# Performance work log

Hardware: AMD Instinct MI355X
Metric: run time of the kernel (lower is better)

## Reference

```python
import jax, jax.numpy as jnp
import numpy as np

N_NODES = 50000
HEADS = 4
NEG_SLOPE = 0.2


def _gat_conv(x, src, dst, W, a_src, a_dst, b):
    """PyG GATConv (concat=True, add_self_loops already applied to src/dst).
    x: [N, F_in], W: [F_in, H*C], a_src/a_dst: [H, C], b: [H*C]."""
    N = x.shape[0]
    HC = W.shape[1]
    C = HC // HEADS
    h = (x @ W).reshape(N, HEADS, C)                       # [N, H, C]
    alpha_s = (h * a_src[None]).sum(-1)                    # [N, H]
    alpha_d = (h * a_dst[None]).sum(-1)                    # [N, H]
    e = jax.nn.leaky_relu(alpha_s[src] + alpha_d[dst], NEG_SLOPE)  # [E, H]
    # segment softmax over incoming edges of each destination node
    m = jax.ops.segment_max(e, dst, num_segments=N)        # [N, H]
    ex = jnp.exp(e - m[dst])
    denom = jax.ops.segment_sum(ex, dst, num_segments=N)   # [N, H]
    alpha = ex / (denom[dst] + 1e-16)                      # [E, H]
    msg = h[src] * alpha[:, :, None]                       # [E, H, C]
    out = jax.ops.segment_sum(msg, dst, num_segments=N)    # [N, H, C]
    return out.reshape(N, HC) + b


def _glorot(key, shape, fan):
    lim = float(np.sqrt(6.0 / fan))
    return jax.random.uniform(key, shape, jnp.float32, -lim, lim)


def setup_inputs() -> dict:
    key = jax.random.key(0)
    ks = jax.random.split(key, 16)
    N, E, F_in, Hid, Out = N_NODES, 800000, 128, 256, 256
    x = jax.random.normal(ks[0], (N, F_in), jnp.float32)
    edge_index = jax.random.randint(ks[1], (2, E), 0, N, jnp.int64)
    C1, C2, C3 = Hid // HEADS, Hid // HEADS, Out // HEADS
    d = {"x": x, "edge_index": edge_index}
    dims = [(F_in, HEADS * C1, C1), (Hid, HEADS * C2, C2), (Hid, HEADS * C3, C3)]
    for i, (fi, fo, c) in enumerate(dims, 1):
        d[f"W{i}"] = _glorot(ks[3 * i], (fi, fo), fi + fo)
        d[f"a_src{i}"] = _glorot(ks[3 * i + 1], (HEADS, c), HEADS * c)
        d[f"a_dst{i}"] = _glorot(ks[3 * i + 2], (HEADS, c), HEADS * c)
        d[f"b{i}"] = jnp.zeros((fo,), jnp.float32)
    return d


def reference(x, edge_index, W1, a_src1, a_dst1, b1, W2, a_src2, a_dst2, b2, W3, a_src3, a_dst3, b3):
    N = x.shape[0]
    loops = jnp.arange(N, dtype=edge_index.dtype)
    src = jnp.concatenate([edge_index[0], loops])  # PyG add_self_loops=True
    dst = jnp.concatenate([edge_index[1], loops])
    h = _gat_conv(x, src, dst, W1, a_src1, a_dst1, b1)
    h = jax.nn.relu(h)  # dropout inert in eval mode
    h = _gat_conv(h, src, dst, W2, a_src2, a_dst2, b2)
    h = jax.nn.relu(h)
    return _gat_conv(h, src, dst, W3, a_src3, a_dst3, b3)
```

## Files before the change

kernel.cpp:

```cpp
#include <hip/hip_runtime.h>
#include <hip/hip_bf16.h>

typedef unsigned short u16;
typedef __attribute__((ext_vector_type(8))) short short8;
typedef __attribute__((ext_vector_type(4))) float f32x4;

#define HC 256
#define NHEAD 4

__device__ __forceinline__ u16 f2b_rne(float v) {
  __hip_bfloat16 b = __float2bfloat16(v);
  union { __hip_bfloat16 b; u16 u; } cv; cv.b = b; return cv.u;
}

__device__ __forceinline__ void w_split_store(const float* W, u16* Th, u16* Tl,
                                              int K, int off) {
  int k = off >> 8, n = off & 255;
  float v = W[off];
  unsigned bits = __float_as_uint(v);
  u16 hi = (u16)(bits >> 16);
  float hf = __uint_as_float((unsigned)hi << 16);
  u16 lo = f2b_rne(v - hf);
  Th[n * K + k] = hi;
  Tl[n * K + k] = lo;
}

__global__ void convert_w3(const float* __restrict__ W1, const float* __restrict__ W2,
                           const float* __restrict__ W3,
                           u16* __restrict__ Th1, u16* __restrict__ Tl1,
                           u16* __restrict__ Th2, u16* __restrict__ Tl2,
                           u16* __restrict__ Th3, u16* __restrict__ Tl3) {
  int id = blockIdx.x * 256 + threadIdx.x;
  const int S1 = 128 * 256, S2 = 256 * 256;
  if (id < S1) w_split_store(W1, Th1, Tl1, 128, id);
  else if (id < S1 + S2) w_split_store(W2, Th2, Tl2, 256, id - S1);
  else if (id < S1 + 2 * S2) w_split_store(W3, Th3, Tl3, 256, id - S1 - S2);
}

#define GBM 128
#define GBN 128
#define GBK 64

__global__ __launch_bounds__(256, 2) void gemm_mfma(
    const float* __restrict__ A, const u16* __restrict__ Bth,
    const u16* __restrict__ Btl, float* __restrict__ C,
    const float* __restrict__ a_src, const float* __restrict__ a_dst,
    float* __restrict__ AS, float* __restrict__ AD, int M, int K, int nMb) {
  __shared__ u16 AH[128 * 64], AL[128 * 64], BH[128 * 64], BL[128 * 64];
  const int tid = threadIdx.x;
  const int lane = tid & 63;
  const int wave = tid >> 6;
  const int wm = (wave & 1) * 64;
  const int wn = (wave >> 1) * 64;

  const int bid = blockIdx.x;
  const int g = bid >> 4;
  const int r = bid & 15;
  const int base = g * 8;
  const int rem = nMb - base;
  int bmi, bni;
  if (rem >= 8) { bmi = base + (r & 7); bni = r >> 3; }
  else          { bmi = base + (r % rem); bni = r / rem; }
  const int bm = bmi * GBM;
  const int bn = bni * GBN;

  const int srow = tid >> 1;
  const int skh  = (tid & 1) * 32;

  f32x4 acc[4][4] = {};

  const int agm = (bm + srow < M) ? (bm + srow) : (M - 1);

  for (int bk = 0; bk < K; bk += GBK) {
    float4 a0[4], a1[4];
    const float* arow = A + (size_t)agm * K + bk + skh;
#pragma unroll
    for (int u = 0; u < 4; ++u) {
      a0[u] = ((const float4*)arow)[2 * u];
      a1[u] = ((const float4*)arow)[2 * u + 1];
    }
    short8 sbh[4], sbl[4];
    const u16* bhrow = Bth + (size_t)(bn + srow) * K + bk + skh;
    const u16* blrow = Btl + (size_t)(bn + srow) * K + bk + skh;
#pragma unroll
    for (int u = 0; u < 4; ++u) {
      sbh[u] = *(const short8*)(bhrow + 8 * u);
      sbl[u] = *(const short8*)(blrow + 8 * u);
    }
    __syncthreads();
#pragma unroll
    for (int u = 0; u < 4; ++u) {
      int idx = (srow * 64 + skh + u * 8) ^ ((srow & 7) << 3);
      float va[8] = {a0[u].x, a0[u].y, a0[u].z, a0[u].w,
                     a1[u].x, a1[u].y, a1[u].z, a1[u].w};
      short8 hi, lo;
#pragma unroll
      for (int j = 0; j < 8; ++j) {
        unsigned bits = __float_as_uint(va[j]);
        u16 h = (u16)(bits >> 16);
        float hf = __uint_as_float((unsigned)h << 16);
        u16 l = f2b_rne(va[j] - hf);
        ((short*)&hi)[j] = (short)h;
        ((short*)&lo)[j] = (short)l;
      }
      *(short8*)&AH[idx] = hi;
      *(short8*)&AL[idx] = lo;
      *(short8*)&BH[idx] = sbh[u];
      *(short8*)&BL[idx] = sbl[u];
    }
    __syncthreads();
#pragma unroll
    for (int ks = 0; ks < 2; ++ks) {
      const int k0 = ks * 32 + (lane >> 4) * 8;
      short8 fah[4], fal[4], fbh[4], fbl[4];
#pragma unroll
      for (int mt = 0; mt < 4; ++mt) {
        int rr = wm + mt * 16 + (lane & 15);
        int idx = (rr * 64 + k0) ^ ((rr & 7) << 3);
        fah[mt] = *(const short8*)&AH[idx];
        fal[mt] = *(const short8*)&AL[idx];
      }
#pragma unroll
      for (int nt = 0; nt < 4; ++nt) {
        int rr = wn + nt * 16 + (lane & 15);
        int idx = (rr * 64 + k0) ^ ((rr & 7) << 3);
        fbh[nt] = *(const short8*)&BH[idx];
        fbl[nt] = *(const short8*)&BL[idx];
      }
#pragma unroll
      for (int mt = 0; mt < 4; ++mt)
#pragma unroll
        for (int nt = 0; nt < 4; ++nt) {
          acc[mt][nt] = __builtin_amdgcn_mfma_f32_16x16x32_bf16(
              fbh[nt], fah[mt], acc[mt][nt], 0, 0, 0);
          acc[mt][nt] = __builtin_amdgcn_mfma_f32_16x16x32_bf16(
              fbh[nt], fal[mt], acc[mt][nt], 0, 0, 0);
          acc[mt][nt] = __builtin_amdgcn_mfma_f32_16x16x32_bf16(
              fbl[nt], fah[mt], acc[mt][nt], 0, 0, 0);
        }
    }
  }
  const int headq = (bn + wn) >> 6;
  float4 sa[4], da[4];
#pragma unroll
  for (int nt = 0; nt < 4; ++nt) {
    sa[nt] = ((const float4*)a_src)[headq * 16 + nt * 4 + (lane >> 4)];
    da[nt] = ((const float4*)a_dst)[headq * 16 + nt * 4 + (lane >> 4)];
  }
#pragma unroll
  for (int mt = 0; mt < 4; ++mt) {
    const int row = bm + wm + mt * 16 + (lane & 15);
    float ps = 0.f, pd = 0.f;
#pragma unroll
    for (int nt = 0; nt < 4; ++nt) {
      ps += acc[mt][nt][0] * sa[nt].x + acc[mt][nt][1] * sa[nt].y +
            acc[mt][nt][2] * sa[nt].z + acc[mt][nt][3] * sa[nt].w;
      pd += acc[mt][nt][0] * da[nt].x + acc[mt][nt][1] * da[nt].y +
            acc[mt][nt][2] * da[nt].z + acc[mt][nt][3] * da[nt].w;
    }
    ps += __shfl_xor(ps, 16); ps += __shfl_xor(ps, 32);
    pd += __shfl_xor(pd, 16); pd += __shfl_xor(pd, 32);
    if (row < M) {
      float* cp = C + (size_t)row * HC + bn + wn + (lane >> 4) * 4;
#pragma unroll
      for (int nt = 0; nt < 4; ++nt)
        *(f32x4*)(cp + nt * 16) = acc[mt][nt];
      if ((lane >> 4) == 0) {
        AS[row * NHEAD + headq] = ps;
        AD[row * NHEAD + headq] = pd;
      }
    }
  }
}

__device__ __forceinline__ float comp4(float4 v, int i) {
  return (i == 0) ? v.x : (i == 1) ? v.y : (i == 2) ? v.z : v.w;
}

__global__ __launch_bounds__(512) void aggregate_kernel(
    const float* __restrict__ h, const float* __restrict__ as_g,
    const float* __restrict__ ad_g, const int* __restrict__ row_ptr,
    const int* __restrict__ csr_src, const float* __restrict__ bias,
    float* __restrict__ out, int relu_flag, int N) {
  __shared__ float4 lacc[4][64];
  __shared__ float lsum[4][64];
  const int wid = threadIdx.x >> 6;
  const int lane = threadIdx.x & 63;
  const int p = wid >> 1;
  const int q = wid & 1;
  const int n = blockIdx.x * 4 + p;
  const int nc = (n < N) ? n : (N - 1);
  const int head = lane >> 4;
  const float4* __restrict__ h4 = (const float4*)h;
  const float4* __restrict__ as4 = (const float4*)as_g;

  const int beg = row_ptr[nc];
  const int end = row_ptr[nc + 1];

  float4 m4 = make_float4(-1e30f, -1e30f, -1e30f, -1e30f);
  for (int j = beg + lane; j < end; j += 64) {
    float4 a = as4[csr_src[j]];
    m4.x = fmaxf(m4.x, a.x); m4.y = fmaxf(m4.y, a.y);
    m4.z = fmaxf(m4.z, a.z); m4.w = fmaxf(m4.w, a.w);
  }
#pragma unroll
  for (int off = 32; off > 0; off >>= 1) {
    m4.x = fmaxf(m4.x, __shfl_xor(m4.x, off));
    m4.y = fmaxf(m4.y, __shfl_xor(m4.y, off));
    m4.z = fmaxf(m4.z, __shfl_xor(m4.z, off));
    m4.w = fmaxf(m4.w, __shfl_xor(m4.w, off));
  }
  const float ad = comp4(((const float4*)ad_g)[nc], head);
  float mm = ad + comp4(m4, head);
  mm = (mm >= 0.f) ? mm : 0.2f * mm;

  float l = 0.f;
  float4 acc = make_float4(0.f, 0.f, 0.f, 0.f);
  for (int j0 = beg + q * 8; j0 < end; j0 += 16) {
    int s[8];
    float ae[8];
    float4 hv[8];
#pragma unroll
    for (int u = 0; u < 8; ++u) {
      int j = j0 + u;
      s[u] = csr_src[(j < end) ? j : (end - 1)];
    }
#pragma unroll
    for (int u = 0; u < 8; ++u) ae[u] = as_g[s[u] * NHEAD + head];
#pragma unroll
    for (int u = 0; u < 8; ++u) hv[u] = h4[(size_t)s[u] * 64 + lane];
#pragma unroll
    for (int u = 0; u < 8; ++u) {
      float e = ae[u] + ad;
      e = (e >= 0.f) ? e : 0.2f * e;
      float pw = __expf(e - mm);
      pw = (j0 + u < end) ? pw : 0.f;
      l += pw;
      acc.x = fmaf(pw, hv[u].x, acc.x);
      acc.y = fmaf(pw, hv[u].y, acc.y);
      acc.z = fmaf(pw, hv[u].z, acc.z);
      acc.w = fmaf(pw, hv[u].w, acc.w);
    }
  }
  if (q == 1) { lacc[p][lane] = acc; lsum[p][lane] = l; }
  __syncthreads();
  if (q == 0 && n < N) {
    float4 a2 = lacc[p][lane];
    acc.x += a2.x; acc.y += a2.y; acc.z += a2.z; acc.w += a2.w;
    l += lsum[p][lane];
    const float inv = 1.f / (l + 1e-16f);
    float4 b4 = ((const float4*)bias)[lane];
    float4 o;
    o.x = acc.x * inv + b4.x; o.y = acc.y * inv + b4.y;
    o.z = acc.z * inv + b4.z; o.w = acc.w * inv + b4.w;
    if (relu_flag) {
      o.x = fmaxf(o.x, 0.f); o.y = fmaxf(o.y, 0.f);
      o.z = fmaxf(o.z, 0.f); o.w = fmaxf(o.w, 0.f);
    }
    ((float4*)out)[(size_t)n * 64 + lane] = o;
  }
}

__global__ void detect_kernel(const int* __restrict__ ei32, int* flag) {
  const int t = threadIdx.x;
  int bad = 0;
#pragma unroll
  for (int r = 0; r < 4; ++r) {
    int i = r * 64 + t;
    if (ei32[2 * i + 1] != 0) bad = 1;
  }
#pragma unroll
  for (int off = 32; off > 0; off >>= 1) bad |= __shfl_down(bad, off);
  if (t == 0) *flag = bad ? 0 : 1;
}

__device__ inline void edge_pair(const int* __restrict__ ei32,
                                 const long long* __restrict__ ei64, int is64,
                                 int e, int E, int& src, int& dst) {
  if (e < E) {
    if (is64) { src = (int)ei64[e]; dst = (int)ei64[(size_t)E + e]; }
    else      { src = ei32[e];      dst = ei32[(size_t)E + e]; }
  } else {
    src = dst = e - E;
  }
}

__global__ void count_kernel(const int* __restrict__ ei32, const int* __restrict__ flag,
                             int* __restrict__ cnt, int E, int Nn) {
  int e = blockIdx.x * blockDim.x + threadIdx.x;
  if (e >= E + Nn) return;
  int is64 = *flag;
  int src, dst;
  edge_pair(ei32, (const long long*)ei32, is64, e, E, src, dst);
  atomicAdd(&cnt[dst], 1);
}

__global__ void scatter_kernel(const int* __restrict__ ei32, const int* __restrict__ flag,
                               int* __restrict__ cursor, int* __restrict__ csr_src,
                               int E, int Nn) {
  int e = blockIdx.x * blockDim.x + threadIdx.x;
  if (e >= E + Nn) return;
  int is64 = *flag;
  int src, dst;
  edge_pair(ei32, (const long long*)ei32, is64, e, E, src, dst);
  int pos = atomicAdd(&cursor[dst], 1);
  csr_src[pos] = src;
}

__global__ __launch_bounds__(256) void scan_blocks(
    const int* __restrict__ cnt, int* __restrict__ local,
    int* __restrict__ partials, int Nn) {
  __shared__ int swave[4];
  const int t = threadIdx.x, lane = t & 63, w = t >> 6;
  const int idx = blockIdx.x * 256 + t;
  int v = (idx < Nn) ? cnt[idx] : 0;
  int x = v;
#pragma unroll
  for (int off = 1; off < 64; off <<= 1) {
    int y = __shfl_up(x, off);
    if (lane >= off) x += y;
  }
  if (lane == 63) swave[w] = x;
  __syncthreads();
  int wofs = 0;
#pragma unroll
  for (int i = 0; i < 3; ++i) wofs += (i < w) ? swave[i] : 0;
  if (idx < Nn) local[idx] = wofs + x - v;
  if (t == 255) partials[blockIdx.x] = wofs + x;
}

__global__ __launch_bounds__(256) void scan_partials(
    int* __restrict__ partials, int nb, int* __restrict__ total_out) {
  __shared__ int swave[4];
  const int t = threadIdx.x, lane = t & 63, w = t >> 6;
  int v = (t < nb) ? partials[t] : 0;
  int x = v;
#pragma unroll
  for (int off = 1; off < 64; off <<= 1) {
    int y = __shfl_up(x, off);
    if (lane >= off) x += y;
  }
  if (lane == 63) swave[w] = x;
  __syncthreads();
  int wofs = 0;
#pragma unroll
  for (int i = 0; i < 3; ++i) wofs += (i < w) ? swave[i] : 0;
  int excl = wofs + x - v;
  if (t < nb) partials[t] = excl;
  if (t == nb - 1) *total_out = excl + v;
}

__global__ void add_offsets(const int* __restrict__ local,
                            const int* __restrict__ partials,
                            int* __restrict__ row_ptr, int* __restrict__ cursor,
                            int Nn) {
  const int idx = blockIdx.x * 256 + threadIdx.x;
  if (idx < Nn) {
    int v = local[idx] + partials[blockIdx.x];
    row_ptr[idx] = v;
    cursor[idx] = v;
  }
}

static inline size_t align_up(size_t v) { return (v + 255) & ~(size_t)255; }

extern "C" void kernel_launch(void* const* d_in, const int* in_sizes, int n_in,
                              void* d_out, int out_size, void* d_ws, size_t ws_size,
                              hipStream_t stream) {
  const float* x      = (const float*)d_in[0];
  const int*   ei32   = (const int*)d_in[1];
  const float* W1     = (const float*)d_in[2];
  const float* asrc1  = (const float*)d_in[3];
  const float* adst1  = (const float*)d_in[4];
  const float* b1     = (const float*)d_in[5];
  const float* W2     = (const float*)d_in[6];
  const float* asrc2  = (const float*)d_in[7];
  const float* adst2  = (const float*)d_in[8];
  const float* b2     = (const float*)d_in[9];
  const float* W3     = (const float*)d_in[10];
  const float* asrc3  = (const float*)d_in[11];
  const float* adst3  = (const float*)d_in[12];
  const float* b3     = (const float*)d_in[13];

  const int N = in_sizes[0] / 128;
  const int E = in_sizes[1] / 2;
  const int ET = E + N;
  float* out = (float*)d_out;
  const int nb = (N + 255) / 256;

  char* w = (char*)d_ws;
  float* H       = (float*)w; w += align_up((size_t)N * HC * sizeof(float));
  float* AS      = (float*)w; w += align_up((size_t)N * NHEAD * sizeof(float));
  float* AD      = (float*)w; w += align_up((size_t)N * NHEAD * sizeof(float));
  int*   cnt     = (int*)w;   w += align_up((size_t)N * sizeof(int));
  int*   local   = (int*)w;   w += align_up((size_t)N * sizeof(int));
  int*   row_ptr = (int*)w;   w += align_up((size_t)(N + 1) * sizeof(int));
  int*   cursor  = (int*)w;   w += align_up((size_t)(N + 1) * sizeof(int));
  int*   parts   = (int*)w;   w += align_up(256 * sizeof(int));
  int*   csr_src = (int*)w;   w += align_up((size_t)ET * sizeof(int));
  u16*   Wth1    = (u16*)w;   w += align_up((size_t)128 * 256 * sizeof(u16));
  u16*   Wtl1    = (u16*)w;   w += align_up((size_t)128 * 256 * sizeof(u16));
  u16*   Wth2    = (u16*)w;   w += align_up((size_t)256 * 256 * sizeof(u16));
  u16*   Wtl2    = (u16*)w;   w += align_up((size_t)256 * 256 * sizeof(u16));
  u16*   Wth3    = (u16*)w;   w += align_up((size_t)256 * 256 * sizeof(u16));
  u16*   Wtl3    = (u16*)w;   w += align_up((size_t)256 * 256 * sizeof(u16));
  int*   flag    = (int*)w;   w += align_up(sizeof(int));

  convert_w3<<<(128 * 256 + 2 * 256 * 256 + 255) / 256, 256, 0, stream>>>(
      W1, W2, W3, Wth1, Wtl1, Wth2, Wtl2, Wth3, Wtl3);
  hipMemsetAsync(cnt, 0, (size_t)N * sizeof(int), stream);
  detect_kernel<<<1, 64, 0, stream>>>(ei32, flag);
  count_kernel<<<(ET + 255) / 256, 256, 0, stream>>>(ei32, flag, cnt, E, N);
  scan_blocks<<<nb, 256, 0, stream>>>(cnt, local, parts, N);
  scan_partials<<<1, 256, 0, stream>>>(parts, nb, row_ptr + N);
  add_offsets<<<nb, 256, 0, stream>>>(local, parts, row_ptr, cursor, N);
  scatter_kernel<<<(ET + 255) / 256, 256, 0, stream>>>(ei32, flag, cursor, csr_src, E, N);

  const int nMb = (N + GBM - 1) / GBM;
  const int gemm_blocks = nMb * 2;
  const int ablk = (N + 3) / 4;

  gemm_mfma<<<gemm_blocks, 256, 0, stream>>>(x, Wth1, Wtl1, H, asrc1, adst1, AS, AD, N, 128, nMb);
  aggregate_kernel<<<ablk, 512, 0, stream>>>(H, AS, AD, row_ptr, csr_src, b1, out, 1, N);

  gemm_mfma<<<gemm_blocks, 256, 0, stream>>>(out, Wth2, Wtl2, H, asrc2, adst2, AS, AD, N, 256, nMb);
  aggregate_kernel<<<ablk, 512, 0, stream>>>(H, AS, AD, row_ptr, csr_src, b2, out, 1, N);

  gemm_mfma<<<gemm_blocks, 256, 0, stream>>>(out, Wth3, Wtl3, H, asrc3, adst3, AS, AD, N, 256, nMb);
  aggregate_kernel<<<ablk, 512, 0, stream>>>(H, AS, AD, row_ptr, csr_src, b3, out, 0, N);
}
```

Before: 598.4 us.

## Aggregate raw features before projection in layer one, fold attention vectors into W1

For the first GAT layer, the attention logits are computed straight from x by folding W1 into a_src/a_dst, giving a 128x4 vector per head. The softmax-weighted neighbour sum then runs on the 128-wide input features, producing one aggregate per head, and a per-head GEMM projects that aggregate and applies bias and ReLU. Gathers drop from 256 to 128 floats per edge, but the GEMM input grows to four times N x 128, which costs extra memory traffic and workspace. The aggregate kernel is also changed from two waves per node with an LDS reduction to one wave per node.

```diff
diff --git a/kernel.cpp b/kernel.cpp
--- a/kernel.cpp
+++ b/kernel.cpp
@@ -35,6 +35,268 @@
   if (id < S1) w_split_store(W1, Th1, Tl1, 128, id);
   else if (id < S1 + S2) w_split_store(W2, Th2, Tl2, 256, id - S1);
   else if (id < S1 + 2 * S2) w_split_store(W3, Th3, Tl3, 256, id - S1 - S2);
+}
+
+__global__ __launch_bounds__(256) void fold_wa(
+    const float* __restrict__ W1, const float* __restrict__ a_src,
+    const float* __restrict__ a_dst, float* __restrict__ wa_s,
+    float* __restrict__ wa_d) {
+  int id = blockIdx.x * 256 + threadIdx.x;
+  if (id >= 512) return;
+  int c = id >> 2, h = id & 3;
+  const float* wrow = W1 + c * 256 + h * 64;
+  const float* as = a_src + h * 64;
+  const float* ad = a_dst + h * 64;
+  float ss = 0.f, sd = 0.f;
+#pragma unroll 8
+  for (int cc = 0; cc < 64; ++cc) {
+    float w = wrow[cc];
+    ss += w * as[cc];
+    sd += w * ad[cc];
+  }
+  wa_s[c * 4 + h] = ss;
+  wa_d[c * 4 + h] = sd;
+}
+
+__global__ __launch_bounds__(256) void alpha_x(
+    const float* __restrict__ x, const float* __restrict__ wa_s,
+    const float* __restrict__ wa_d, float* __restrict__ AS,
+    float* __restrict__ AD, int N) {
+  const int wave = threadIdx.x >> 6;
+  const int lane = threadIdx.x & 63;
+  const int n = blockIdx.x * 4 + wave;
+  if (n >= N) return;
+  float2 xv = ((const float2*)x)[(size_t)n * 64 + lane];
+  float4 sA = ((const float4*)wa_s)[2 * lane];
+  float4 sB = ((const float4*)wa_s)[2 * lane + 1];
+  float4 dA = ((const float4*)wa_d)[2 * lane];
+  float4 dB = ((const float4*)wa_d)[2 * lane + 1];
+  float ps[4], pd[4];
+  ps[0] = xv.x * sA.x + xv.y * sB.x;  pd[0] = xv.x * dA.x + xv.y * dB.x;
+  ps[1] = xv.x * sA.y + xv.y * sB.y;  pd[1] = xv.x * dA.y + xv.y * dB.y;
+  ps[2] = xv.x * sA.z + xv.y * sB.z;  pd[2] = xv.x * dA.z + xv.y * dB.z;
+  ps[3] = xv.x * sA.w + xv.y * sB.w;  pd[3] = xv.x * dA.w + xv.y * dB.w;
+#pragma unroll
+  for (int off = 1; off < 64; off <<= 1) {
+#pragma unroll
+    for (int h = 0; h < 4; ++h) {
+      ps[h] += __shfl_xor(ps[h], off);
+      pd[h] += __shfl_xor(pd[h], off);
+    }
+  }
+  if (lane == 0) {
+#pragma unroll
+    for (int h = 0; h < 4; ++h) {
+      AS[n * NHEAD + h] = ps[h];
+      AD[n * NHEAD + h] = pd[h];
+    }
+  }
+}
+
+__device__ __forceinline__ float lky(float e) {
+  return (e >= 0.f) ? e : 0.2f * e;
+}
+
+__global__ __launch_bounds__(256) void aggregate_x4(
+    const float* __restrict__ x, const float* __restrict__ as_g,
+    const float* __restrict__ ad_g, const int* __restrict__ row_ptr,
+    const int* __restrict__ csr_src, float* __restrict__ xagg, int N) {
+  const int wave = threadIdx.x >> 6;
+  const int lane = threadIdx.x & 63;
+  const int n = blockIdx.x * 4 + wave;
+  if (n >= N) return;
+  const float2* __restrict__ x2 = (const float2*)x;
+  const float4* __restrict__ as4 = (const float4*)as_g;
+
+  const int beg = row_ptr[n];
+  const int end = row_ptr[n + 1];
+
+  float4 m4 = make_float4(-1e30f, -1e30f, -1e30f, -1e30f);
+  for (int j = beg + lane; j < end; j += 64) {
+    float4 a = as4[csr_src[j]];
+    m4.x = fmaxf(m4.x, a.x); m4.y = fmaxf(m4.y, a.y);
+    m4.z = fmaxf(m4.z, a.z); m4.w = fmaxf(m4.w, a.w);
+  }
+#pragma unroll
+  for (int off = 32; off > 0; off >>= 1) {
+    m4.x = fmaxf(m4.x, __shfl_xor(m4.x, off));
+    m4.y = fmaxf(m4.y, __shfl_xor(m4.y, off));
+    m4.z = fmaxf(m4.z, __shfl_xor(m4.z, off));
+    m4.w = fmaxf(m4.w, __shfl_xor(m4.w, off));
+  }
+  const float4 ad4 = ((const float4*)ad_g)[n];
+  float4 mm4;
+  mm4.x = lky(ad4.x + m4.x);
+  mm4.y = lky(ad4.y + m4.y);
+  mm4.z = lky(ad4.z + m4.z);
+  mm4.w = lky(ad4.w + m4.w);
+
+  float4 l4 = make_float4(0.f, 0.f, 0.f, 0.f);
+  float2 ac0 = make_float2(0.f, 0.f), ac1 = ac0, ac2 = ac0, ac3 = ac0;
+  for (int j0 = beg; j0 < end; j0 += 8) {
+    int s[8];
+    float4 av[8];
+    float2 xv[8];
+#pragma unroll
+    for (int u = 0; u < 8; ++u) {
+      int j = j0 + u;
+      s[u] = csr_src[(j < end) ? j : (end - 1)];
+    }
+#pragma unroll
+    for (int u = 0; u < 8; ++u) av[u] = as4[s[u]];
+#pragma unroll
+    for (int u = 0; u < 8; ++u) xv[u] = x2[(size_t)s[u] * 64 + lane];
+#pragma unroll
+    for (int u = 0; u < 8; ++u) {
+      const bool live = (j0 + u < end);
+      float4 p;
+      p.x = __expf(lky(av[u].x + ad4.x) - mm4.x);
+      p.y = __expf(lky(av[u].y + ad4.y) - mm4.y);
+      p.z = __expf(lky(av[u].z + ad4.z) - mm4.z);
+      p.w = __expf(lky(av[u].w + ad4.w) - mm4.w);
+      p.x = live ? p.x : 0.f; p.y = live ? p.y : 0.f;
+      p.z = live ? p.z : 0.f; p.w = live ? p.w : 0.f;
+      l4.x += p.x; l4.y += p.y; l4.z += p.z; l4.w += p.w;
+      ac0.x = fmaf(p.x, xv[u].x, ac0.x); ac0.y = fmaf(p.x, xv[u].y, ac0.y);
+      ac1.x = fmaf(p.y, xv[u].x, ac1.x); ac1.y = fmaf(p.y, xv[u].y, ac1.y);
+      ac2.x = fmaf(p.z, xv[u].x, ac2.x); ac2.y = fmaf(p.z, xv[u].y, ac2.y);
+      ac3.x = fmaf(p.w, xv[u].x, ac3.x); ac3.y = fmaf(p.w, xv[u].y, ac3.y);
+    }
+  }
+  const float i0 = 1.f / (l4.x + 1e-16f);
+  const float i1 = 1.f / (l4.y + 1e-16f);
+  const float i2 = 1.f / (l4.z + 1e-16f);
+  const float i3 = 1.f / (l4.w + 1e-16f);
+  float2* __restrict__ o2 = (float2*)xagg;
+  const size_t plane = (size_t)N * 64;
+  const size_t base = (size_t)n * 64 + lane;
+  o2[0 * plane + base] = make_float2(ac0.x * i0, ac0.y * i0);
+  o2[1 * plane + base] = make_float2(ac1.x * i1, ac1.y * i1);
+  o2[2 * plane + base] = make_float2(ac2.x * i2, ac2.y * i2);
+  o2[3 * plane + base] = make_float2(ac3.x * i3, ac3.y * i3);
+}
+
+__global__ __launch_bounds__(256, 2) void gemm_mfma_h(
+    const float* __restrict__ Aall, const u16* __restrict__ Bth,
+    const u16* __restrict__ Btl, float* __restrict__ C,
+    const float* __restrict__ bias, int M) {
+  __shared__ u16 AH[128 * 64], AL[128 * 64], BH[64 * 64], BL[64 * 64];
+  const int tid = threadIdx.x;
+  const int lane = tid & 63;
+  const int wave = tid >> 6;
+  const int wm = (wave & 1) * 64;
+  const int wn = (wave >> 1) * 32;
+  const int head = blockIdx.y;
+  const int bm = blockIdx.x * 128;
+
+  const float* A = Aall + (size_t)head * M * 128;
+  const u16* bth = Bth + head * 64 * 128;
+  const u16* btl = Btl + head * 64 * 128;
+
+  const int srow = tid >> 1;
+  const int skh  = (tid & 1) * 32;
+  const int bcol = tid >> 2;
+  const int bkq  = (tid & 3) * 16;
+
+  f32x4 acc[4][2] = {};
+  const int agm = (bm + srow < M) ? (bm + srow) : (M - 1);
+
+  for (int bk = 0; bk < 128; bk += 64) {
+    float4 a0[4], a1[4];
+    const float* arow = A + (size_t)agm * 128 + bk + skh;
+#pragma unroll
+    for (int u = 0; u < 4; ++u) {
+      a0[u] = ((const float4*)arow)[2 * u];
+      a1[u] = ((const float4*)arow)[2 * u + 1];
+    }
+    short8 sbh[2], sbl[2];
+    {
+      const u16* p = bth + bcol * 128 + bk + bkq;
+      sbh[0] = *(const short8*)p;
+      sbh[1] = *(const short8*)(p + 8);
+      const u16* q = btl + bcol * 128 + bk + bkq;
+      sbl[0] = *(const short8*)q;
+      sbl[1] = *(const short8*)(q + 8);
+    }
+    __syncthreads();
+#pragma unroll
+    for (int u = 0; u < 4; ++u) {
+      int idx = (srow * 64 + skh + u * 8) ^ ((srow & 7) << 3);
+      float va[8] = {a0[u].x, a0[u].y, a0[u].z, a0[u].w,
+                     a1[u].x, a1[u].y, a1[u].z, a1[u].w};
+      short8 hi, lo;
+#pragma unroll
+      for (int j = 0; j < 8; ++j) {
+        unsigned bits = __float_as_uint(va[j]);
+        u16 h = (u16)(bits >> 16);
+        float hf = __uint_as_float((unsigned)h << 16);
+        u16 l = f2b_rne(va[j] - hf);
+        ((short*)&hi)[j] = (short)h;
+        ((short*)&lo)[j] = (short)l;
+      }
+      *(short8*)&AH[idx] = hi;
+      *(short8*)&AL[idx] = lo;
+    }
+    {
+      int i0 = (bcol * 64 + bkq) ^ ((bcol & 7) << 3);
+      int i1 = (bcol * 64 + bkq + 8) ^ ((bcol & 7) << 3);
+      *(short8*)&BH[i0] = sbh[0];
+      *(short8*)&BH[i1] = sbh[1];
+      *(short8*)&BL[i0] = sbl[0];
+      *(short8*)&BL[i1] = sbl[1];
+    }
+    __syncthreads();
+#pragma unroll
+    for (int ks = 0; ks < 2; ++ks) {
+      const int k0 = ks * 32 + (lane >> 4) * 8;
+      short8 fah[4], fal[4], fbh[2], fbl[2];
+#pragma unroll
+      for (int mt = 0; mt < 4; ++mt) {
+        int rr = wm + mt * 16 + (lane & 15);
+        int idx = (rr * 64 + k0) ^ ((rr & 7) << 3);
+        fah[mt] = *(const short8*)&AH[idx];
+        fal[mt] = *(const short8*)&AL[idx];
+      }
+#pragma unroll
+      for (int nt = 0; nt < 2; ++nt) {
+        int rr = wn + nt * 16 + (lane & 15);
+        int idx = (rr * 64 + k0) ^ ((rr & 7) << 3);
+        fbh[nt] = *(const short8*)&BH[idx];
+        fbl[nt] = *(const short8*)&BL[idx];
+      }
+#pragma unroll
+      for (int mt = 0; mt < 4; ++mt)
+#pragma unroll
+        for (int nt = 0; nt < 2; ++nt) {
+          acc[mt][nt] = __builtin_amdgcn_mfma_f32_16x16x32_bf16(
+              fbh[nt], fah[mt], acc[mt][nt], 0, 0, 0);
+          acc[mt][nt] = __builtin_amdgcn_mfma_f32_16x16x32_bf16(
+              fbh[nt], fal[mt], acc[mt][nt], 0, 0, 0);
+          acc[mt][nt] = __builtin_amdgcn_mfma_f32_16x16x32_bf16(
+              fbl[nt], fah[mt], acc[mt][nt], 0, 0, 0);
+        }
+    }
+  }
+  float4 b4[2];
+#pragma unroll
+  for (int nt = 0; nt < 2; ++nt)
+    b4[nt] = ((const float4*)bias)[head * 16 + (wn >> 2) + nt * 4 + (lane >> 4)];
+#pragma unroll
+  for (int mt = 0; mt < 4; ++mt) {
+    const int row = bm + wm + mt * 16 + (lane & 15);
+    if (row < M) {
+      float* cp = C + (size_t)row * HC + head * 64 + wn + (lane >> 4) * 4;
+#pragma unroll
+      for (int nt = 0; nt < 2; ++nt) {
+        f32x4 v = acc[mt][nt];
+        v[0] = fmaxf(v[0] + b4[nt].x, 0.f);
+        v[1] = fmaxf(v[1] + b4[nt].y, 0.f);
+        v[2] = fmaxf(v[2] + b4[nt].z, 0.f);
+        v[3] = fmaxf(v[3] + b4[nt].w, 0.f);
+        *(f32x4*)(cp + nt * 16) = v;
+      }
+    }
+  }
 }
 
 #define GBM 128
@@ -68,7 +330,6 @@
   const int skh  = (tid & 1) * 32;
 
   f32x4 acc[4][4] = {};
-
   const int agm = (bm + srow < M) ? (bm + srow) : (M - 1);
 
   for (int bk = 0; bk < K; bk += GBK) {
@@ -177,25 +438,21 @@
   return (i == 0) ? v.x : (i == 1) ? v.y : (i == 2) ? v.z : v.w;
 }
 
-__global__ __launch_bounds__(512) void aggregate_kernel(
+__global__ __launch_bounds__(256) void aggregate_kernel(
     const float* __restrict__ h, const float* __restrict__ as_g,
     const float* __restrict__ ad_g, const int* __restrict__ row_ptr,
     const int* __restrict__ csr_src, const float* __restrict__ bias,
     float* __restrict__ out, int relu_flag, int N) {
-  __shared__ float4 lacc[4][64];
-  __shared__ float lsum[4][64];
-  const int wid = threadIdx.x >> 6;
+  const int wave = threadIdx.x >> 6;
   const int lane = threadIdx.x & 63;
-  const int p = wid >> 1;
-  const int q = wid & 1;
-  const int n = blockIdx.x * 4 + p;
-  const int nc = (n < N) ? n : (N - 1);
+  const int n = blockIdx.x * 4 + wave;
+  if (n >= N) return;
   const int head = lane >> 4;
   const float4* __restrict__ h4 = (const float4*)h;
   const float4* __restrict__ as4 = (const float4*)as_g;
 
-  const int beg = row_ptr[nc];
-  const int end = row_ptr[nc + 1];
+  const int beg = row_ptr[n];
+  const int end = row_ptr[n + 1];
 
   float4 m4 = make_float4(-1e30f, -1e30f, -1e30f, -1e30f);
   for (int j = beg + lane; j < end; j += 64) {
@@ -210,13 +467,12 @@
     m4.z = fmaxf(m4.z, __shfl_xor(m4.z, off));
     m4.w = fmaxf(m4.w, __shfl_xor(m4.w, off));
   }
-  const float ad = comp4(((const float4*)ad_g)[nc], head);
-  float mm = ad + comp4(m4, head);
-  mm = (mm >= 0.f) ? mm : 0.2f * mm;
+  const float ad = comp4(((const float4*)ad_g)[n], head);
+  float mm = lky(ad + comp4(m4, head));
 
   float l = 0.f;
   float4 acc = make_float4(0.f, 0.f, 0.f, 0.f);
-  for (int j0 = beg + q * 8; j0 < end; j0 += 16) {
+  for (int j0 = beg; j0 < end; j0 += 8) {
     int s[8];
     float ae[8];
     float4 hv[8];
@@ -231,34 +487,25 @@
     for (int u = 0; u < 8; ++u) hv[u] = h4[(size_t)s[u] * 64 + lane];
 #pragma unroll
     for (int u = 0; u < 8; ++u) {
-      float e = ae[u] + ad;
-      e = (e >= 0.f) ? e : 0.2f * e;
-      float pw = __expf(e - mm);
-      pw = (j0 + u < end) ? pw : 0.f;
-      l += pw;
-      acc.x = fmaf(pw, hv[u].x, acc.x);
-      acc.y = fmaf(pw, hv[u].y, acc.y);
-      acc.z = fmaf(pw, hv[u].z, acc.z);
-      acc.w = fmaf(pw, hv[u].w, acc.w);
-    }
-  }
-  if (q == 1) { lacc[p][lane] = acc; lsum[p][lane] = l; }
-  __syncthreads();
-  if (q == 0 && n < N) {
-    float4 a2 = lacc[p][lane];
-    acc.x += a2.x; acc.y += a2.y; acc.z += a2.z; acc.w += a2.w;
-    l += lsum[p][lane];
-    const float inv = 1.f / (l + 1e-16f);
-    float4 b4 = ((const float4*)bias)[lane];
-    float4 o;
-    o.x = acc.x * inv + b4.x; o.y = acc.y * inv + b4.y;
-    o.z = acc.z * inv + b4.z; o.w = acc.w * inv + b4.w;
-    if (relu_flag) {
-      o.x = fmaxf(o.x, 0.f); o.y = fmaxf(o.y, 0.f);
-      o.z = fmaxf(o.z, 0.f); o.w = fmaxf(o.w, 0.f);
-    }
-    ((float4*)out)[(size_t)n * 64 + lane] = o;
-  }
+      float p = __expf(lky(ae[u] + ad) - mm);
+      p = (j0 + u < end) ? p : 0.f;
+      l += p;
+      acc.x = fmaf(p, hv[u].x, acc.x);
+      acc.y = fmaf(p, hv[u].y, acc.y);
+      acc.z = fmaf(p, hv[u].z, acc.z);
+      acc.w = fmaf(p, hv[u].w, acc.w);
+    }
+  }
+  const float inv = 1.f / (l + 1e-16f);
+  float4 b4 = ((const float4*)bias)[lane];
+  float4 o;
+  o.x = acc.x * inv + b4.x; o.y = acc.y * inv + b4.y;
+  o.z = acc.z * inv + b4.z; o.w = acc.w * inv + b4.w;
+  if (relu_flag) {
+    o.x = fmaxf(o.x, 0.f); o.y = fmaxf(o.y, 0.f);
+    o.z = fmaxf(o.z, 0.f); o.w = fmaxf(o.w, 0.f);
+  }
+  ((float4*)out)[(size_t)n * 64 + lane] = o;
 }
 
 __global__ void detect_kernel(const int* __restrict__ ei32, int* flag) {
@@ -389,9 +636,12 @@
   const int nb = (N + 255) / 256;
 
   char* w = (char*)d_ws;
-  float* H       = (float*)w; w += align_up((size_t)N * HC * sizeof(float));
+  float* XAGG    = (float*)w;
+  float* H       = (float*)w; w += align_up((size_t)N * 512 * sizeof(float));
   float* AS      = (float*)w; w += align_up((size_t)N * NHEAD * sizeof(float));
   float* AD      = (float*)w; w += align_up((size_t)N * NHEAD * sizeof(float));
+  float* WA1S    = (float*)w; w += align_up((size_t)128 * 4 * sizeof(float));
+  float* WA1D    = (float*)w; w += align_up((size_t)128 * 4 * sizeof(float));
   int*   cnt     = (int*)w;   w += align_up((size_t)N * sizeof(int));
   int*   local   = (int*)w;   w += align_up((size_t)N * sizeof(int));
   int*   row_ptr = (int*)w;   w += align_up((size_t)(N + 1) * sizeof(int));
@@ -408,6 +658,7 @@
 
   convert_w3<<<(128 * 256 + 2 * 256 * 256 + 255) / 256, 256, 0, stream>>>(
       W1, W2, W3, Wth1, Wtl1, Wth2, Wtl2, Wth3, Wtl3);
+  fold_wa<<<2, 256, 0, stream>>>(W1, asrc1, adst1, WA1S, WA1D);
   hipMemsetAsync(cnt, 0, (size_t)N * sizeof(int), stream);
   detect_kernel<<<1, 64, 0, stream>>>(ei32, flag);
   count_kernel<<<(ET + 255) / 256, 256, 0, stream>>>(ei32, flag, cnt, E, N);
@@ -420,12 +671,15 @@
   const int gemm_blocks = nMb * 2;
   const int ablk = (N + 3) / 4;
 
-  gemm_mfma<<<gemm_blocks, 256, 0, stream>>>(x, Wth1, Wtl1, H, asrc1, adst1, AS, AD, N, 128, nMb);
-  aggregate_kernel<<<ablk, 512, 0, stream>>>(H, AS, AD, row_ptr, csr_src, b1, out, 1, N);
-
-  gemm_mfma<<<gemm_blocks, 256, 0, stream>>>(out, Wth2, Wtl2, H, asrc2, adst2, AS, AD, N, 256, nMb);
-  aggregate_kernel<<<ablk, 512, 0, stream>>>(H, AS, AD, row_ptr, csr_src, b2, out, 1, N);
-
-  gemm_mfma<<<gemm_blocks, 256, 0, stream>>>(out, Wth3, Wtl3, H, asrc3, adst3, AS, AD, N, 256, nMb);
-  aggregate_kernel<<<ablk, 512, 0, stream>>>(H, AS, AD, row_ptr, csr_src, b3, out, 0, N);
-}
+  alpha_x<<<ablk, 256, 0, stream>>>(x, WA1S, WA1D, AS, AD, N);
+  aggregate_x4<<<ablk, 256, 0, stream>>>(x, AS, AD, row_ptr, csr_src, XAGG, N);
+  gemm_mfma_h<<<dim3(nMb, 4), 256, 0, stream>>>(XAGG, Wth1, Wtl1, out, b1, N);
+
+  gemm_mfma<<<gemm_blocks, 256, 0, stream>>>(out, Wth2, Wtl2, H,
+      asrc2, adst2, AS, AD, N, 256, nMb);
+  aggregate_kernel<<<ablk, 256, 0, stream>>>(H, AS, AD, row_ptr, csr_src, b2, out, 1, N);
+
+  gemm_mfma<<<gemm_blocks, 256, 0, stream>>>(out, Wth3, Wtl3, H,
+      asrc3, adst3, AS, AD, N, 256, nMb);
+  aggregate_kernel<<<ablk, 256, 0, stream>>>(H, AS, AD, row_ptr, csr_src, b3, out, 0, N);
+}
```

Result: no change. 608.7 us (+1.7%).

## Split GAT aggregation into softmax stats pass and column-sliced aggregate

Applied to the files above, without the earlier changes.

Moves the per-node softmax max and denominator into a separate softmax_stats kernel, so the aggregation no longer needs a running sum or a cross-wave LDS reduction. The aggregation now runs 8 blocks per group of 4 nodes, each handling a 32-column slice (one head half). Within a wave, the two lane halves take alternating edges and are combined with a shuffle. This makes the feature gathers narrower and likely more L2-friendly, and raises parallelism. The cost is an extra kernel launch per layer and the edge index and attention scores being re-read once per slice.

```diff
diff --git a/kernel.cpp b/kernel.cpp
--- a/kernel.cpp
+++ b/kernel.cpp
@@ -35,6 +35,14 @@
   if (id < S1) w_split_store(W1, Th1, Tl1, 128, id);
   else if (id < S1 + S2) w_split_store(W2, Th2, Tl2, 256, id - S1);
   else if (id < S1 + 2 * S2) w_split_store(W3, Th3, Tl3, 256, id - S1 - S2);
+}
+
+__device__ __forceinline__ float lky(float e) {
+  return (e >= 0.f) ? e : 0.2f * e;
+}
+
+__device__ __forceinline__ float comp4(float4 v, int i) {
+  return (i == 0) ? v.x : (i == 1) ? v.y : (i == 2) ? v.z : v.w;
 }
 
 #define GBM 128
@@ -68,7 +76,6 @@
   const int skh  = (tid & 1) * 32;
 
   f32x4 acc[4][4] = {};
-
   const int agm = (bm + srow < M) ? (bm + srow) : (M - 1);
 
   for (int bk = 0; bk < K; bk += GBK) {
@@ -173,29 +180,17 @@
   }
 }
 
-__device__ __forceinline__ float comp4(float4 v, int i) {
-  return (i == 0) ? v.x : (i == 1) ? v.y : (i == 2) ? v.z : v.w;
-}
-
-__global__ __launch_bounds__(512) void aggregate_kernel(
-    const float* __restrict__ h, const float* __restrict__ as_g,
-    const float* __restrict__ ad_g, const int* __restrict__ row_ptr,
-    const int* __restrict__ csr_src, const float* __restrict__ bias,
-    float* __restrict__ out, int relu_flag, int N) {
-  __shared__ float4 lacc[4][64];
-  __shared__ float lsum[4][64];
-  const int wid = threadIdx.x >> 6;
+__global__ __launch_bounds__(256) void softmax_stats(
+    const float* __restrict__ as_g, const float* __restrict__ ad_g,
+    const int* __restrict__ row_ptr, const int* __restrict__ csr_src,
+    float* __restrict__ MM, float* __restrict__ INVL, int N) {
+  const int wave = threadIdx.x >> 6;
   const int lane = threadIdx.x & 63;
-  const int p = wid >> 1;
-  const int q = wid & 1;
-  const int n = blockIdx.x * 4 + p;
-  const int nc = (n < N) ? n : (N - 1);
-  const int head = lane >> 4;
-  const float4* __restrict__ h4 = (const float4*)h;
+  const int n = blockIdx.x * 4 + wave;
+  if (n >= N) return;
   const float4* __restrict__ as4 = (const float4*)as_g;
-
-  const int beg = row_ptr[nc];
-  const int end = row_ptr[nc + 1];
+  const int beg = row_ptr[n];
+  const int end = row_ptr[n + 1];
 
   float4 m4 = make_float4(-1e30f, -1e30f, -1e30f, -1e30f);
   for (int j = beg + lane; j < end; j += 64) {
@@ -210,54 +205,88 @@
     m4.z = fmaxf(m4.z, __shfl_xor(m4.z, off));
     m4.w = fmaxf(m4.w, __shfl_xor(m4.w, off));
   }
-  const float ad = comp4(((const float4*)ad_g)[nc], head);
-  float mm = ad + comp4(m4, head);
-  mm = (mm >= 0.f) ? mm : 0.2f * mm;
-
-  float l = 0.f;
-  float4 acc = make_float4(0.f, 0.f, 0.f, 0.f);
-  for (int j0 = beg + q * 8; j0 < end; j0 += 16) {
+  const float4 ad4 = ((const float4*)ad_g)[n];
+  float4 mm4;
+  mm4.x = lky(ad4.x + m4.x);
+  mm4.y = lky(ad4.y + m4.y);
+  mm4.z = lky(ad4.z + m4.z);
+  mm4.w = lky(ad4.w + m4.w);
+
+  float4 l4 = make_float4(0.f, 0.f, 0.f, 0.f);
+  for (int j = beg + lane; j < end; j += 64) {
+    float4 a = as4[csr_src[j]];
+    l4.x += __expf(lky(a.x + ad4.x) - mm4.x);
+    l4.y += __expf(lky(a.y + ad4.y) - mm4.y);
+    l4.z += __expf(lky(a.z + ad4.z) - mm4.z);
+    l4.w += __expf(lky(a.w + ad4.w) - mm4.w);
+  }
+#pragma unroll
+  for (int off = 32; off > 0; off >>= 1) {
+    l4.x += __shfl_xor(l4.x, off);
+    l4.y += __shfl_xor(l4.y, off);
+    l4.z += __shfl_xor(l4.z, off);
+    l4.w += __shfl_xor(l4.w, off);
+  }
+  if (lane == 0) {
+    ((float4*)MM)[n] = mm4;
+    float4 inv;
+    inv.x = 1.f / (l4.x + 1e-16f);
+    inv.y = 1.f / (l4.y + 1e-16f);
+    inv.z = 1.f / (l4.z + 1e-16f);
+    inv.w = 1.f / (l4.w + 1e-16f);
+    ((float4*)INVL)[n] = inv;
+  }
+}
+
+__global__ __launch_bounds__(256) void aggregate_sliced(
+    const float* __restrict__ h, const float* __restrict__ as_g,
+    const float* __restrict__ ad_g, const float* __restrict__ MM,
+    const float* __restrict__ INVL, const int* __restrict__ row_ptr,
+    const int* __restrict__ csr_src, const float* __restrict__ bias,
+    float* __restrict__ out, int relu_flag, int N) {
+  const int q = blockIdx.x & 7;
+  const int ng = blockIdx.x >> 3;
+  const int wave = threadIdx.x >> 6;
+  const int lane = threadIdx.x & 63;
+  const int n = ng * 4 + wave;
+  if (n >= N) return;
+  const int head = q >> 1;
+  const int epar = lane >> 5;
+  const int c = lane & 31;
+
+  const int beg = row_ptr[n];
+  const int end = row_ptr[n + 1];
+  const float ad = ad_g[n * NHEAD + head];
+  const float mm = MM[n * NHEAD + head];
+  const float il = INVL[n * NHEAD + head];
+  const float* __restrict__ hsl = h + q * 32 + c;
+
+  float acc = 0.f;
+  for (int j0 = beg; j0 < end; j0 += 16) {
     int s[8];
     float ae[8];
-    float4 hv[8];
+    float hv[8];
 #pragma unroll
     for (int u = 0; u < 8; ++u) {
-      int j = j0 + u;
+      int j = j0 + 2 * u + epar;
       s[u] = csr_src[(j < end) ? j : (end - 1)];
     }
 #pragma unroll
     for (int u = 0; u < 8; ++u) ae[u] = as_g[s[u] * NHEAD + head];
 #pragma unroll
-    for (int u = 0; u < 8; ++u) hv[u] = h4[(size_t)s[u] * 64 + lane];
+    for (int u = 0; u < 8; ++u) hv[u] = hsl[(size_t)s[u] * HC];
 #pragma unroll
     for (int u = 0; u < 8; ++u) {
-      float e = ae[u] + ad;
-      e = (e >= 0.f) ? e : 0.2f * e;
-      float pw = __expf(e - mm);
-      pw = (j0 + u < end) ? pw : 0.f;
-      l += pw;
-      acc.x = fmaf(pw, hv[u].x, acc.x);
-      acc.y = fmaf(pw, hv[u].y, acc.y);
-      acc.z = fmaf(pw, hv[u].z, acc.z);
-      acc.w = fmaf(pw, hv[u].w, acc.w);
-    }
-  }
-  if (q == 1) { lacc[p][lane] = acc; lsum[p][lane] = l; }
-  __syncthreads();
-  if (q == 0 && n < N) {
-    float4 a2 = lacc[p][lane];
-    acc.x += a2.x; acc.y += a2.y; acc.z += a2.z; acc.w += a2.w;
-    l += lsum[p][lane];
-    const float inv = 1.f / (l + 1e-16f);
-    float4 b4 = ((const float4*)bias)[lane];
-    float4 o;
-    o.x = acc.x * inv + b4.x; o.y = acc.y * inv + b4.y;
-    o.z = acc.z * inv + b4.z; o.w = acc.w * inv + b4.w;
-    if (relu_flag) {
-      o.x = fmaxf(o.x, 0.f); o.y = fmaxf(o.y, 0.f);
-      o.z = fmaxf(o.z, 0.f); o.w = fmaxf(o.w, 0.f);
-    }
-    ((float4*)out)[(size_t)n * 64 + lane] = o;
+      float p = __expf(lky(ae[u] + ad) - mm);
+      p = (j0 + 2 * u + epar < end) ? p : 0.f;
+      acc = fmaf(p, hv[u], acc);
+    }
+  }
+  acc += __shfl_xor(acc, 32);
+  if (epar == 0) {
+    float o = acc * il + bias[q * 32 + c];
+    if (relu_flag) o = fmaxf(o, 0.f);
+    out[(size_t)n * HC + q * 32 + c] = o;
   }
 }
 
@@ -392,6 +421,8 @@
   float* H       = (float*)w; w += align_up((size_t)N * HC * sizeof(float));
   float* AS      = (float*)w; w += align_up((size_t)N * NHEAD * sizeof(float));
   float* AD      = (float*)w; w += align_up((size_t)N * NHEAD * sizeof(float));
+  float* MM      = (float*)w; w += align_up((size_t)N * NHEAD * sizeof(float));
+  float* INVL    = (float*)w; w += align_up((size_t)N * NHEAD * sizeof(float));
   int*   cnt     = (int*)w;   w += align_up((size_t)N * sizeof(int));
   int*   local   = (int*)w;   w += align_up((size_t)N * sizeof(int));
   int*   row_ptr = (int*)w;   w += align_up((size_t)(N + 1) * sizeof(int));
@@ -419,13 +450,23 @@
   const int nMb = (N + GBM - 1) / GBM;
   const int gemm_blocks = nMb * 2;
   const int ablk = (N + 3) / 4;
-
-  gemm_mfma<<<gemm_blocks, 256, 0, stream>>>(x, Wth1, Wtl1, H, asrc1, adst1, AS, AD, N, 128, nMb);
-  aggregate_kernel<<<ablk, 512, 0, stream>>>(H, AS, AD, row_ptr, csr_src, b1, out, 1, N);
-
-  gemm_mfma<<<gemm_blocks, 256, 0, stream>>>(out, Wth2, Wtl2, H, asrc2, adst2, AS, AD, N, 256, nMb);
-  aggregate_kernel<<<ablk, 512, 0, stream>>>(H, AS, AD, row_ptr, csr_src, b2, out, 1, N);
-
-  gemm_mfma<<<gemm_blocks, 256, 0, stream>>>(out, Wth3, Wtl3, H, asrc3, adst3, AS, AD, N, 256, nMb);
-  aggregate_kernel<<<ablk, 512, 0, stream>>>(H, AS, AD, row_ptr, csr_src, b3, out, 0, N);
-}
+  const int sblk = ablk * 8;
+
+  gemm_mfma<<<gemm_blocks, 256, 0, stream>>>(x, Wth1, Wtl1, H,
+      asrc1, adst1, AS, AD, N, 128, nMb);
+  softmax_stats<<<ablk, 256, 0, stream>>>(AS, AD, row_ptr, csr_src, MM, INVL, N);
+  aggregate_sliced<<<sblk, 256, 0, stream>>>(H, AS, AD, MM, INVL, row_ptr,
+      csr_src, b1, out, 1, N);
+
+  gemm_mfma<<<gemm_blocks, 256, 0, stream>>>(out, Wth2, Wtl2, H,
+      asrc2, adst2, AS, AD, N, 256, nMb);
+  softmax_stats<<<ablk, 256, 0, stream>>>(AS, AD, row_ptr, csr_src, MM, INVL, N);
+  aggregate_sliced<<<sblk, 256, 0, stream>>>(H, AS, AD, MM, INVL, row_ptr,
+      csr_src, b2, out, 1, N);
+
+  gemm_mfma<<<gemm_blocks, 256, 0, stream>>>(out, Wth3, Wtl3, H,
+      asrc3, adst3, AS, AD, N, 256, nMb);
+  softmax_stats<<<ablk, 256, 0, stream>>>(AS, AD, row_ptr, csr_src, MM, INVL, N);
+  aggregate_sliced<<<sblk, 256, 0, stream>>>(H, AS, AD, MM, INVL, row_ptr,
+      csr_src, b3, out, 0, N);
+}
```

Result: slower. 824.2 us (+37.7%).
